# Kernel optimization log

Hardware: AMD Instinct MI355X
Metric: run time of the kernel (lower is better)

Reference implementation:

```python
import jax, jax.numpy as jnp
import numpy as np

N, KS, C = 1_000_000, 9, 16
EPS = 1e-5
SLOPE = 0.2  # LeakyReLU negative_slope


def _leaky(x):
    return jnp.where(x >= 0, x, SLOPE * x)


def _batchnorm(x, gamma, beta):
    # BatchNorm1d in training mode: biased batch statistics over the N axis
    mean = x.mean(axis=0)
    var = x.var(axis=0)
    return gamma * (x - mean) * jax.lax.rsqrt(var + EPS) + beta


def setup_inputs() -> dict:
    key = jax.random.key(0)
    k = jax.random.split(key, 5)
    xav = (2.0 / (C + C)) ** 0.5  # xavier-normal-ish scale for [C_in, C_out, ks]
    return {
        "data": jax.random.normal(k[0], (N, C), jnp.float32),
        "ind": jax.random.randint(k[1], (N, KS), 0, N),
        "w1": jax.random.normal(k[2], (C, C, KS), jnp.float32) * xav,
        "b1": jax.random.normal(k[3], (C,), jnp.float32) * 0.01,
        "gamma1": jnp.ones((C,), jnp.float32),
        "beta1": jnp.zeros((C,), jnp.float32),
        "w2": jax.random.normal(k[4], (C, C, KS), jnp.float32) * xav,
        "gamma2": jnp.ones((C,), jnp.float32),
        "beta2": jnp.zeros((C,), jnp.float32),
    }


def reference(data, ind, w1, b1, gamma1, beta1, w2, gamma2, beta2):
    # gather neighborhoods: [N, ks, C]
    inp = data[ind]
    # torch.einsum('ijk,klj->il', data[N,ks,C], weight[C,Cout,ks]) -> [N, Cout]
    out = jnp.einsum('njc,coj->no', inp, w1) + b1
    out = _leaky(_batchnorm(out, gamma1, beta1))
    # second gather + tree-conv, no bias
    out = jnp.einsum('njc,coj->no', out[ind], w2)
    out = _batchnorm(out, gamma2, beta2)
    # residual (in_channels == out_channels -> identity shortcut)
    return _leaky(out + data)
```

## Files before the change

### kernel.cpp

```cpp
#include <hip/hip_runtime.h>

typedef unsigned int uint;
typedef unsigned short ushort;

#define NN 1000000
#define KSZ 9
#define CH 16
#define KTOT 144
#define NBLK 1024
#define TILES64 15625

typedef float f32x4 __attribute__((ext_vector_type(4)));
typedef short s16x8 __attribute__((ext_vector_type(8)));

__device__ __forceinline__ float bf2f(ushort v) { return __uint_as_float(((uint)v) << 16); }
__device__ __forceinline__ ushort f2bf(float f) {
  uint u = __float_as_uint(f);
  return (ushort)((u + 0x7fffu + ((u >> 16) & 1u)) >> 16);
}
__device__ __forceinline__ float leaky(float x) { return x >= 0.f ? x : 0.2f * x; }

__global__ __launch_bounds__(256)
void k_cast(const float* __restrict__ in, ushort* __restrict__ out) {
  size_t i0 = ((size_t)blockIdx.x * 256 + (size_t)threadIdx.x) * 8;
  if (i0 >= (size_t)NN * CH) return;
  float4 a = *(const float4*)(in + i0);
  float4 b = *(const float4*)(in + i0 + 4);
  float e[8] = {a.x, a.y, a.z, a.w, b.x, b.y, b.z, b.w};
  uint pk[4];
#pragma unroll
  for (int p = 0; p < 4; ++p)
    pk[p] = (uint)f2bf(e[2*p]) | ((uint)f2bf(e[2*p+1]) << 16);
  *(uint4*)(out + i0) = *(uint4*)pk;
}

template<bool BN>
__global__ __launch_bounds__(256)
void k_conv(const ushort* __restrict__ src, const int* __restrict__ ind,
            const float* __restrict__ w, const float* __restrict__ bias,
            const float* __restrict__ statsIn, const float* __restrict__ gamma,
            const float* __restrict__ beta,
            ushort* __restrict__ outv, float* __restrict__ accumOut) {
  const int lane = threadIdx.x & 63;
  const int wid  = threadIdx.x >> 6;
  const int o = lane & 15;
  const int q = lane >> 4;
  const int qh = q >> 1;
  const int ch0 = (q & 1) * 8;

  __shared__ int   idxs[4][160];
  __shared__ float red[4][32];
  __shared__ float dsc[16], dsh[16];

  s16x8 bfrag[5];
#pragma unroll
  for (int t = 0; t < 5; ++t) {
#pragma unroll
    for (int i = 0; i < 8; ++i) {
      int k = t * 32 + q * 8 + i;
      ushort wv = 0;
      if (k < KTOT) { int j = k >> 4, c = k & 15; wv = f2bf(w[(c * CH + o) * KSZ + j]); }
      bfrag[t][i] = (short)wv;
    }
  }

  float bo = 0.f;
  float sc8[8], sh8[8];
  if constexpr (BN) {
    if (threadIdx.x < 16) {
      int c = threadIdx.x;
      float s = statsIn[c], sq = statsIn[16 + c];
      float mean = s * (1.0f / NN);
      float var  = sq * (1.0f / NN) - mean * mean;
      float scale = gamma[c] * rsqrtf(var + 1e-5f);
      dsc[c] = scale; dsh[c] = beta[c] - mean * scale;
    }
    __syncthreads();
#pragma unroll
    for (int i = 0; i < 8; ++i) { sc8[i] = dsc[ch0 + i]; sh8[i] = dsh[ch0 + i]; }
  } else {
    bo = bias[o];
  }

  int* idxw = idxs[wid];
  float wsum = 0.f, wsq = 0.f;

  for (int g = blockIdx.x; g < TILES64; g += NBLK) {
    const int base  = g * 64 + wid * 16;
    const int base9 = base * 9;

    {
      int r = lane;            idxw[r] = ind[base9 + r];
      r = lane + 64;           idxw[r] = ind[base9 + r];
      r = lane + 128; if (r < KTOT) idxw[r] = ind[base9 + r];
    }

    int i0 = idxw[o * KSZ + (0 + qh)];
    int i1 = idxw[o * KSZ + (2 + qh)];
    int i2 = idxw[o * KSZ + (4 + qh)];
    int i3 = idxw[o * KSZ + (6 + qh)];
    int i4 = idxw[o * KSZ + 8];

    const ushort* p0 = src + (size_t)i0 * CH + ch0;
    const ushort* p1 = src + (size_t)i1 * CH + ch0;
    const ushort* p2 = src + (size_t)i2 * CH + ch0;
    const ushort* p3 = src + (size_t)i3 * CH + ch0;
    const ushort* p4 = src + (size_t)i4 * CH + ch0;

    s16x8 ld0, ld1, ld2, ld3, ld4;
    asm volatile("global_load_dwordx4 %0, %1, off sc0" : "=&v"(ld0) : "v"(p0) : "memory");
    asm volatile("global_load_dwordx4 %0, %1, off sc0" : "=&v"(ld1) : "v"(p1) : "memory");
    asm volatile("global_load_dwordx4 %0, %1, off sc0" : "=&v"(ld2) : "v"(p2) : "memory");
    asm volatile("global_load_dwordx4 %0, %1, off sc0" : "=&v"(ld3) : "v"(p3) : "memory");
    asm volatile("global_load_dwordx4 %0, %1, off sc0" : "=&v"(ld4) : "v"(p4) : "memory");
    asm volatile("s_waitcnt vmcnt(0)" ::: "memory");
    __builtin_amdgcn_sched_barrier(0);

    s16x8 a0, a1, a2, a3, a4;
    if constexpr (BN) {
      auto xf = [&](s16x8 v) -> s16x8 {
        s16x8 r;
#pragma unroll
        for (int i = 0; i < 8; ++i) {
          float x = bf2f((ushort)v[i]);
          r[i] = (short)f2bf(leaky(sc8[i] * x + sh8[i]));
        }
        return r;
      };
      a0 = xf(ld0); a1 = xf(ld1); a2 = xf(ld2); a3 = xf(ld3); a4 = xf(ld4);
    } else {
      a0 = ld0; a1 = ld1; a2 = ld2; a3 = ld3; a4 = ld4;
    }
    if (qh) { s16x8 z = {0,0,0,0,0,0,0,0}; a4 = z; }

    f32x4 acc = {0.f, 0.f, 0.f, 0.f};
    acc = __builtin_amdgcn_mfma_f32_16x16x32_bf16(a0, bfrag[0], acc, 0, 0, 0);
    acc = __builtin_amdgcn_mfma_f32_16x16x32_bf16(a1, bfrag[1], acc, 0, 0, 0);
    acc = __builtin_amdgcn_mfma_f32_16x16x32_bf16(a2, bfrag[2], acc, 0, 0, 0);
    acc = __builtin_amdgcn_mfma_f32_16x16x32_bf16(a3, bfrag[3], acc, 0, 0, 0);
    acc = __builtin_amdgcn_mfma_f32_16x16x32_bf16(a4, bfrag[4], acc, 0, 0, 0);

#pragma unroll
    for (int r = 0; r < 4; ++r) {
      float v = acc[r] + bo;
      ushort hv = f2bf(v);
      outv[(size_t)(base + q * 4 + r) * CH + o] = hv;
      float vr = bf2f(hv);
      wsum += vr;
      wsq  += vr * vr;
    }
  }

  wsum += __shfl_xor(wsum, 16);  wsum += __shfl_xor(wsum, 32);
  wsq  += __shfl_xor(wsq, 16);   wsq  += __shfl_xor(wsq, 32);
  if (lane < 16) { red[wid][lane] = wsum; red[wid][16 + lane] = wsq; }
  __syncthreads();
  if (threadIdx.x < 32) {
    float s = red[0][threadIdx.x] + red[1][threadIdx.x] + red[2][threadIdx.x] + red[3][threadIdx.x];
    atomicAdd(&accumOut[threadIdx.x], s);
  }
}

__global__ __launch_bounds__(256)
void k_final(const ushort* __restrict__ o2, const float* __restrict__ data,
             const float* __restrict__ statsIn, const float* __restrict__ gamma,
             const float* __restrict__ beta, float* __restrict__ out) {
  __shared__ float dsc[16], dsh[16];
  if (threadIdx.x < 16) {
    int c = threadIdx.x;
    float s = statsIn[c], sq = statsIn[16 + c];
    float mean = s * (1.0f / NN);
    float var  = sq * (1.0f / NN) - mean * mean;
    float scale = gamma[c] * rsqrtf(var + 1e-5f);
    dsc[c] = scale; dsh[c] = beta[c] - mean * scale;
  }
  __syncthreads();
  size_t t = (size_t)blockIdx.x * 256 + threadIdx.x;
  size_t i0 = t * 8;
  if (i0 >= (size_t)NN * CH) return;
  int coff = (int)(i0 & 15);
  float sc[8], sh[8];
#pragma unroll
  for (int p = 0; p < 8; ++p) { sc[p] = dsc[coff + p]; sh[p] = dsh[coff + p]; }
  uint4 a = *(const uint4*)(o2 + i0);
  float4 d0 = *(const float4*)(data + i0);
  float4 d1 = *(const float4*)(data + i0 + 4);
  uint ua[4] = {a.x, a.y, a.z, a.w};
  float dd[8] = {d0.x, d0.y, d0.z, d0.w, d1.x, d1.y, d1.z, d1.w};
  float y[8];
#pragma unroll
  for (int p = 0; p < 4; ++p) {
    float x0 = __uint_as_float(ua[p] << 16);
    float x1 = __uint_as_float(ua[p] & 0xffff0000u);
    y[2*p]   = leaky(sc[2*p]   * x0 + sh[2*p]   + dd[2*p]);
    y[2*p+1] = leaky(sc[2*p+1] * x1 + sh[2*p+1] + dd[2*p+1]);
  }
  float4 r0 = {y[0], y[1], y[2], y[3]};
  float4 r1 = {y[4], y[5], y[6], y[7]};
  *(float4*)(out + i0) = r0;
  *(float4*)(out + i0 + 4) = r1;
}

extern "C" void kernel_launch(void* const* d_in, const int* in_sizes, int n_in,
                              void* d_out, int out_size, void* d_ws, size_t ws_size,
                              hipStream_t stream) {
  const float* data   = (const float*)d_in[0];
  const int*   ind    = (const int*)d_in[1];
  const float* w1     = (const float*)d_in[2];
  const float* b1     = (const float*)d_in[3];
  const float* gamma1 = (const float*)d_in[4];
  const float* beta1  = (const float*)d_in[5];
  const float* w2     = (const float*)d_in[6];
  const float* gamma2 = (const float*)d_in[7];
  const float* beta2  = (const float*)d_in[8];
  float* out = (float*)d_out;

  ushort* out1  = (ushort*)d_out;
  ushort* dataB = out1 + (size_t)NN * CH;
  float*  accum1 = (float*)d_ws;
  float*  accum2 = accum1 + 32;
  ushort* out2   = (ushort*)((char*)d_ws + 256);

  hipMemsetAsync(d_ws, 0, 256, stream);

  hipLaunchKernelGGL(k_cast, dim3((NN * CH / 8 + 255) / 256), dim3(256), 0, stream,
                     data, dataB);
  hipLaunchKernelGGL((k_conv<false>), dim3(NBLK), dim3(256), 0, stream,
                     dataB, ind, w1, b1,
                     (const float*)nullptr, (const float*)nullptr, (const float*)nullptr,
                     out1, accum1);
  hipLaunchKernelGGL((k_conv<true>), dim3(NBLK), dim3(256), 0, stream,
                     out1, ind, w2, (const float*)nullptr,
                     accum1, gamma1, beta1,
                     out2, accum2);
  hipLaunchKernelGGL(k_final, dim3((NN * CH / 8 + 255) / 256), dim3(256), 0, stream,
                     out2, data, accum2, gamma2, beta2, out);
}
```

Before: 471.6 us.

## Partition gathers into index-range passes with soft grid barriers for cache locality

Each conv kernel now caches all of a block's tile indices in shared memory and keeps 16 accumulators per wave. It sweeps the source array in 8 index-range windows (index >> 17), with a bounded-spin soft barrier across blocks before each pass. Each pass only loads the gathered rows that fall in the current window, so the working set of random gathers can stay in L2/MALL. The BN+leaky transform on layer-1 output moves out of the second conv into a separate in-place elementwise kernel, so the conv is one template again. In exchange, every tile is revisited 8 times, register pressure rises, barrier spinning costs time, and there is an extra pass over the intermediate tensor.

Result: slower. 1.256 ms (+166.3%).

```diff
diff --git a/kernel.cpp b/kernel.cpp
--- a/kernel.cpp
+++ b/kernel.cpp
@@ -9,6 +9,9 @@
 #define KTOT 144
 #define NBLK 1024
 #define TILES64 15625
+#define MAXT 16
+#define WSHIFT 17
+#define NPASS 8
 
 typedef float f32x4 __attribute__((ext_vector_type(4)));
 typedef short s16x8 __attribute__((ext_vector_type(8)));
@@ -19,6 +22,18 @@
   return (ushort)((u + 0x7fffu + ((u >> 16) & 1u)) >> 16);
 }
 __device__ __forceinline__ float leaky(float x) { return x >= 0.f ? x : 0.2f * x; }
+
+__device__ __forceinline__ void soft_barrier(int* bar, int wp) {
+  __syncthreads();
+  if (threadIdx.x == 0) {
+    __hip_atomic_fetch_add(&bar[wp], 1, __ATOMIC_RELAXED, __HIP_MEMORY_SCOPE_AGENT);
+    int tries = 0;
+    while (__hip_atomic_load(&bar[wp], __ATOMIC_RELAXED, __HIP_MEMORY_SCOPE_AGENT) < NBLK
+           && ++tries < 96)
+      __builtin_amdgcn_s_sleep(8);
+  }
+  __syncthreads();
+}
 
 __global__ __launch_bounds__(256)
 void k_cast(const float* __restrict__ in, ushort* __restrict__ out) {
@@ -34,13 +49,11 @@
   *(uint4*)(out + i0) = *(uint4*)pk;
 }
 
-template<bool BN>
-__global__ __launch_bounds__(256)
+__global__ __launch_bounds__(256, 4)
 void k_conv(const ushort* __restrict__ src, const int* __restrict__ ind,
             const float* __restrict__ w, const float* __restrict__ bias,
-            const float* __restrict__ statsIn, const float* __restrict__ gamma,
-            const float* __restrict__ beta,
-            ushort* __restrict__ outv, float* __restrict__ accumOut) {
+            ushort* __restrict__ outv, float* __restrict__ accumOut,
+            int* __restrict__ bar) {
   const int lane = threadIdx.x & 63;
   const int wid  = threadIdx.x >> 6;
   const int o = lane & 15;
@@ -48,9 +61,8 @@
   const int qh = q >> 1;
   const int ch0 = (q & 1) * 8;
 
-  __shared__ int   idxs[4][160];
+  __shared__ int   idxs[4][MAXT][KTOT];
   __shared__ float red[4][32];
-  __shared__ float dsc[16], dsh[16];
 
   s16x8 bfrag[5];
 #pragma unroll
@@ -64,85 +76,67 @@
     }
   }
 
-  float bo = 0.f;
-  float sc8[8], sh8[8];
-  if constexpr (BN) {
-    if (threadIdx.x < 16) {
-      int c = threadIdx.x;
-      float s = statsIn[c], sq = statsIn[16 + c];
-      float mean = s * (1.0f / NN);
-      float var  = sq * (1.0f / NN) - mean * mean;
-      float scale = gamma[c] * rsqrtf(var + 1e-5f);
-      dsc[c] = scale; dsh[c] = beta[c] - mean * scale;
-    }
-    __syncthreads();
-#pragma unroll
-    for (int i = 0; i < 8; ++i) { sc8[i] = dsc[ch0 + i]; sh8[i] = dsh[ch0 + i]; }
-  } else {
-    bo = bias[o];
-  }
-
-  int* idxw = idxs[wid];
+  float bo = bias ? bias[o] : 0.f;
+
+#pragma unroll
+  for (int tt = 0; tt < MAXT; ++tt) {
+    int g = blockIdx.x + tt * NBLK;
+    if (g < TILES64) {
+      int base9 = (g * 64 + wid * 16) * 9;
+      idxs[wid][tt][lane]      = ind[base9 + lane];
+      idxs[wid][tt][lane + 64] = ind[base9 + lane + 64];
+      if (lane < KTOT - 128) idxs[wid][tt][lane + 128] = ind[base9 + lane + 128];
+    }
+  }
+
+  f32x4 acc[MAXT];
+#pragma unroll
+  for (int tt = 0; tt < MAXT; ++tt) acc[tt] = (f32x4){0.f, 0.f, 0.f, 0.f};
+
+  for (int wp = 0; wp < NPASS; ++wp) {
+    soft_barrier(bar, wp);
+#pragma unroll
+    for (int tt = 0; tt < MAXT; ++tt) {
+      int g = blockIdx.x + tt * NBLK;
+      if (g >= TILES64) continue;
+      const int* tix = idxs[wid][tt];
+      int i0 = tix[o * KSZ + 0 + qh];
+      int i1 = tix[o * KSZ + 2 + qh];
+      int i2 = tix[o * KSZ + 4 + qh];
+      int i3 = tix[o * KSZ + 6 + qh];
+      int i4 = tix[o * KSZ + 8];
+      const ushort* p0 = src + (size_t)i0 * CH + ch0;
+      const ushort* p1 = src + (size_t)i1 * CH + ch0;
+      const ushort* p2 = src + (size_t)i2 * CH + ch0;
+      const ushort* p3 = src + (size_t)i3 * CH + ch0;
+      const ushort* p4 = src + (size_t)i4 * CH + ch0;
+      s16x8 z = {0,0,0,0,0,0,0,0};
+      s16x8 a0 = z, a1 = z, a2 = z, a3 = z, a4 = z;
+      if ((i0 >> WSHIFT) == wp) asm volatile("global_load_dwordx4 %0, %1, off sc0" : "+v"(a0) : "v"(p0) : "memory");
+      if ((i1 >> WSHIFT) == wp) asm volatile("global_load_dwordx4 %0, %1, off sc0" : "+v"(a1) : "v"(p1) : "memory");
+      if ((i2 >> WSHIFT) == wp) asm volatile("global_load_dwordx4 %0, %1, off sc0" : "+v"(a2) : "v"(p2) : "memory");
+      if ((i3 >> WSHIFT) == wp) asm volatile("global_load_dwordx4 %0, %1, off sc0" : "+v"(a3) : "v"(p3) : "memory");
+      if (qh == 0 && (i4 >> WSHIFT) == wp)
+        asm volatile("global_load_dwordx4 %0, %1, off sc0" : "+v"(a4) : "v"(p4) : "memory");
+      asm volatile("s_waitcnt vmcnt(0)" ::: "memory");
+      __builtin_amdgcn_sched_barrier(0);
+      acc[tt] = __builtin_amdgcn_mfma_f32_16x16x32_bf16(a0, bfrag[0], acc[tt], 0, 0, 0);
+      acc[tt] = __builtin_amdgcn_mfma_f32_16x16x32_bf16(a1, bfrag[1], acc[tt], 0, 0, 0);
+      acc[tt] = __builtin_amdgcn_mfma_f32_16x16x32_bf16(a2, bfrag[2], acc[tt], 0, 0, 0);
+      acc[tt] = __builtin_amdgcn_mfma_f32_16x16x32_bf16(a3, bfrag[3], acc[tt], 0, 0, 0);
+      acc[tt] = __builtin_amdgcn_mfma_f32_16x16x32_bf16(a4, bfrag[4], acc[tt], 0, 0, 0);
+    }
+  }
+
   float wsum = 0.f, wsq = 0.f;
-
-  for (int g = blockIdx.x; g < TILES64; g += NBLK) {
-    const int base  = g * 64 + wid * 16;
-    const int base9 = base * 9;
-
-    {
-      int r = lane;            idxw[r] = ind[base9 + r];
-      r = lane + 64;           idxw[r] = ind[base9 + r];
-      r = lane + 128; if (r < KTOT) idxw[r] = ind[base9 + r];
-    }
-
-    int i0 = idxw[o * KSZ + (0 + qh)];
-    int i1 = idxw[o * KSZ + (2 + qh)];
-    int i2 = idxw[o * KSZ + (4 + qh)];
-    int i3 = idxw[o * KSZ + (6 + qh)];
-    int i4 = idxw[o * KSZ + 8];
-
-    const ushort* p0 = src + (size_t)i0 * CH + ch0;
-    const ushort* p1 = src + (size_t)i1 * CH + ch0;
-    const ushort* p2 = src + (size_t)i2 * CH + ch0;
-    const ushort* p3 = src + (size_t)i3 * CH + ch0;
-    const ushort* p4 = src + (size_t)i4 * CH + ch0;
-
-    s16x8 ld0, ld1, ld2, ld3, ld4;
-    asm volatile("global_load_dwordx4 %0, %1, off sc0" : "=&v"(ld0) : "v"(p0) : "memory");
-    asm volatile("global_load_dwordx4 %0, %1, off sc0" : "=&v"(ld1) : "v"(p1) : "memory");
-    asm volatile("global_load_dwordx4 %0, %1, off sc0" : "=&v"(ld2) : "v"(p2) : "memory");
-    asm volatile("global_load_dwordx4 %0, %1, off sc0" : "=&v"(ld3) : "v"(p3) : "memory");
-    asm volatile("global_load_dwordx4 %0, %1, off sc0" : "=&v"(ld4) : "v"(p4) : "memory");
-    asm volatile("s_waitcnt vmcnt(0)" ::: "memory");
-    __builtin_amdgcn_sched_barrier(0);
-
-    s16x8 a0, a1, a2, a3, a4;
-    if constexpr (BN) {
-      auto xf = [&](s16x8 v) -> s16x8 {
-        s16x8 r;
-#pragma unroll
-        for (int i = 0; i < 8; ++i) {
-          float x = bf2f((ushort)v[i]);
-          r[i] = (short)f2bf(leaky(sc8[i] * x + sh8[i]));
-        }
-        return r;
-      };
-      a0 = xf(ld0); a1 = xf(ld1); a2 = xf(ld2); a3 = xf(ld3); a4 = xf(ld4);
-    } else {
-      a0 = ld0; a1 = ld1; a2 = ld2; a3 = ld3; a4 = ld4;
-    }
-    if (qh) { s16x8 z = {0,0,0,0,0,0,0,0}; a4 = z; }
-
-    f32x4 acc = {0.f, 0.f, 0.f, 0.f};
-    acc = __builtin_amdgcn_mfma_f32_16x16x32_bf16(a0, bfrag[0], acc, 0, 0, 0);
-    acc = __builtin_amdgcn_mfma_f32_16x16x32_bf16(a1, bfrag[1], acc, 0, 0, 0);
-    acc = __builtin_amdgcn_mfma_f32_16x16x32_bf16(a2, bfrag[2], acc, 0, 0, 0);
-    acc = __builtin_amdgcn_mfma_f32_16x16x32_bf16(a3, bfrag[3], acc, 0, 0, 0);
-    acc = __builtin_amdgcn_mfma_f32_16x16x32_bf16(a4, bfrag[4], acc, 0, 0, 0);
-
+#pragma unroll
+  for (int tt = 0; tt < MAXT; ++tt) {
+    int g = blockIdx.x + tt * NBLK;
+    if (g >= TILES64) continue;
+    int base = g * 64 + wid * 16;
 #pragma unroll
     for (int r = 0; r < 4; ++r) {
-      float v = acc[r] + bo;
+      float v = acc[tt][r] + bo;
       ushort hv = f2bf(v);
       outv[(size_t)(base + q * 4 + r) * CH + o] = hv;
       float vr = bf2f(hv);
@@ -159,6 +153,39 @@
     float s = red[0][threadIdx.x] + red[1][threadIdx.x] + red[2][threadIdx.x] + red[3][threadIdx.x];
     atomicAdd(&accumOut[threadIdx.x], s);
   }
+}
+
+__global__ __launch_bounds__(256)
+void k_bn(ushort* __restrict__ io, const float* __restrict__ statsIn,
+          const float* __restrict__ gamma, const float* __restrict__ beta) {
+  __shared__ float dsc[16], dsh[16];
+  if (threadIdx.x < 16) {
+    int c = threadIdx.x;
+    float s = statsIn[c], sq = statsIn[16 + c];
+    float mean = s * (1.0f / NN);
+    float var  = sq * (1.0f / NN) - mean * mean;
+    float scale = gamma[c] * rsqrtf(var + 1e-5f);
+    dsc[c] = scale; dsh[c] = beta[c] - mean * scale;
+  }
+  __syncthreads();
+  size_t i0 = ((size_t)blockIdx.x * 256 + (size_t)threadIdx.x) * 8;
+  if (i0 >= (size_t)NN * CH) return;
+  int coff = (int)(i0 & 15);
+  float sc[8], sh[8];
+#pragma unroll
+  for (int p = 0; p < 8; ++p) { sc[p] = dsc[coff + p]; sh[p] = dsh[coff + p]; }
+  uint4 a = *(const uint4*)(io + i0);
+  uint ua[4] = {a.x, a.y, a.z, a.w};
+  uint pk[4];
+#pragma unroll
+  for (int p = 0; p < 4; ++p) {
+    float x0 = __uint_as_float(ua[p] << 16);
+    float x1 = __uint_as_float(ua[p] & 0xffff0000u);
+    float y0 = leaky(sc[2*p]   * x0 + sh[2*p]);
+    float y1 = leaky(sc[2*p+1] * x1 + sh[2*p+1]);
+    pk[p] = (uint)f2bf(y0) | ((uint)f2bf(y1) << 16);
+  }
+  *(uint4*)(io + i0) = *(uint4*)pk;
 }
 
 __global__ __launch_bounds__(256)
@@ -219,20 +246,24 @@
   ushort* dataB = out1 + (size_t)NN * CH;
   float*  accum1 = (float*)d_ws;
   float*  accum2 = accum1 + 32;
-  ushort* out2   = (ushort*)((char*)d_ws + 256);
-
-  hipMemsetAsync(d_ws, 0, 256, stream);
+  int*    bar1   = (int*)((char*)d_ws + 256);
+  int*    bar2   = bar1 + 8;
+  ushort* out2   = (ushort*)((char*)d_ws + 4096);
+
+  hipMemsetAsync(d_ws, 0, 512, stream);
 
   hipLaunchKernelGGL(k_cast, dim3((NN * CH / 8 + 255) / 256), dim3(256), 0, stream,
                      data, dataB);
-  hipLaunchKernelGGL((k_conv<false>), dim3(NBLK), dim3(256), 0, stream,
-                     dataB, ind, w1, b1,
-                     (const float*)nullptr, (const float*)nullptr, (const float*)nullptr,
-                     out1, accum1);
-  hipLaunchKernelGGL((k_conv<true>), dim3(NBLK), dim3(256), 0, stream,
-                     out1, ind, w2, (const float*)nullptr,
-                     accum1, gamma1, beta1,
-                     out2, accum2);
+
+  hipLaunchKernelGGL(k_conv, dim3(NBLK), dim3(256), 0, stream,
+                     dataB, ind, w1, b1, out1, accum1, bar1);
+
+  hipLaunchKernelGGL(k_bn, dim3((NN * CH / 8 + 255) / 256), dim3(256), 0, stream,
+                     out1, accum1, gamma1, beta1);
+
+  hipLaunchKernelGGL(k_conv, dim3(NBLK), dim3(256), 0, stream,
+                     out1, ind, w2, (const float*)nullptr, out2, accum2, bar2);
+
   hipLaunchKernelGGL(k_final, dim3((NN * CH / 8 + 255) / 256), dim3(256), 0, stream,
                      out2, data, accum2, gamma2, beta2, out);
 }
```

## Fuse fp32-to-bf16 cast into first conv gather and double block count

Applied to the files above, without the earlier changes.

Drops the separate cast kernel. The first conv now gathers the fp32 rows directly, using two 16-byte loads per neighbor, and packs them to bf16 with v_cvt_pk_bf16_f32 in registers. This removes one full pass over the input and the write of a bf16 copy, but the first conv's random gathers now move twice as many bytes. The grid-stride block count is also raised from 1024 to 2048, and the out2 workspace offset moves to 4096.

Result: no change. 471.2 us (-0.1%).

```diff
diff --git a/kernel.cpp b/kernel.cpp
--- a/kernel.cpp
+++ b/kernel.cpp
@@ -7,7 +7,7 @@
 #define KSZ 9
 #define CH 16
 #define KTOT 144
-#define NBLK 1024
+#define NBLK 2048
 #define TILES64 15625
 
 typedef float f32x4 __attribute__((ext_vector_type(4)));
@@ -20,23 +20,9 @@
 }
 __device__ __forceinline__ float leaky(float x) { return x >= 0.f ? x : 0.2f * x; }
 
+template<bool FP32SRC>
 __global__ __launch_bounds__(256)
-void k_cast(const float* __restrict__ in, ushort* __restrict__ out) {
-  size_t i0 = ((size_t)blockIdx.x * 256 + (size_t)threadIdx.x) * 8;
-  if (i0 >= (size_t)NN * CH) return;
-  float4 a = *(const float4*)(in + i0);
-  float4 b = *(const float4*)(in + i0 + 4);
-  float e[8] = {a.x, a.y, a.z, a.w, b.x, b.y, b.z, b.w};
-  uint pk[4];
-#pragma unroll
-  for (int p = 0; p < 4; ++p)
-    pk[p] = (uint)f2bf(e[2*p]) | ((uint)f2bf(e[2*p+1]) << 16);
-  *(uint4*)(out + i0) = *(uint4*)pk;
-}
-
-template<bool BN>
-__global__ __launch_bounds__(256)
-void k_conv(const ushort* __restrict__ src, const int* __restrict__ ind,
+void k_conv(const void* __restrict__ srcv, const int* __restrict__ ind,
             const float* __restrict__ w, const float* __restrict__ bias,
             const float* __restrict__ statsIn, const float* __restrict__ gamma,
             const float* __restrict__ beta,
@@ -47,6 +33,7 @@
   const int q = lane >> 4;
   const int qh = q >> 1;
   const int ch0 = (q & 1) * 8;
+  const int o9 = o * KSZ;
 
   __shared__ int   idxs[4][160];
   __shared__ float red[4][32];
@@ -66,7 +53,9 @@
 
   float bo = 0.f;
   float sc8[8], sh8[8];
-  if constexpr (BN) {
+  if constexpr (FP32SRC) {
+    bo = bias[o];
+  } else {
     if (threadIdx.x < 16) {
       int c = threadIdx.x;
       float s = statsIn[c], sq = statsIn[16 + c];
@@ -78,8 +67,6 @@
     __syncthreads();
 #pragma unroll
     for (int i = 0; i < 8; ++i) { sc8[i] = dsc[ch0 + i]; sh8[i] = dsh[ch0 + i]; }
-  } else {
-    bo = bias[o];
   }
 
   int* idxw = idxs[wid];
@@ -89,35 +76,63 @@
     const int base  = g * 64 + wid * 16;
     const int base9 = base * 9;
 
-    {
-      int r = lane;            idxw[r] = ind[base9 + r];
-      r = lane + 64;           idxw[r] = ind[base9 + r];
-      r = lane + 128; if (r < KTOT) idxw[r] = ind[base9 + r];
-    }
-
-    int i0 = idxw[o * KSZ + (0 + qh)];
-    int i1 = idxw[o * KSZ + (2 + qh)];
-    int i2 = idxw[o * KSZ + (4 + qh)];
-    int i3 = idxw[o * KSZ + (6 + qh)];
-    int i4 = idxw[o * KSZ + 8];
-
-    const ushort* p0 = src + (size_t)i0 * CH + ch0;
-    const ushort* p1 = src + (size_t)i1 * CH + ch0;
-    const ushort* p2 = src + (size_t)i2 * CH + ch0;
-    const ushort* p3 = src + (size_t)i3 * CH + ch0;
-    const ushort* p4 = src + (size_t)i4 * CH + ch0;
-
-    s16x8 ld0, ld1, ld2, ld3, ld4;
-    asm volatile("global_load_dwordx4 %0, %1, off sc0" : "=&v"(ld0) : "v"(p0) : "memory");
-    asm volatile("global_load_dwordx4 %0, %1, off sc0" : "=&v"(ld1) : "v"(p1) : "memory");
-    asm volatile("global_load_dwordx4 %0, %1, off sc0" : "=&v"(ld2) : "v"(p2) : "memory");
-    asm volatile("global_load_dwordx4 %0, %1, off sc0" : "=&v"(ld3) : "v"(p3) : "memory");
-    asm volatile("global_load_dwordx4 %0, %1, off sc0" : "=&v"(ld4) : "v"(p4) : "memory");
-    asm volatile("s_waitcnt vmcnt(0)" ::: "memory");
-    __builtin_amdgcn_sched_barrier(0);
+    idxw[lane]      = ind[base9 + lane];
+    idxw[lane + 64] = ind[base9 + lane + 64];
+    if (lane < KTOT - 128) idxw[lane + 128] = ind[base9 + lane + 128];
+
+    int i0 = idxw[o9 + 0 + qh];
+    int i1 = idxw[o9 + 2 + qh];
+    int i2 = idxw[o9 + 4 + qh];
+    int i3 = idxw[o9 + 6 + qh];
+    int i4 = idxw[o9 + 8];
 
     s16x8 a0, a1, a2, a3, a4;
-    if constexpr (BN) {
+    if constexpr (FP32SRC) {
+      const float* fsrc = (const float*)srcv;
+      const float* p0 = fsrc + (size_t)i0 * CH + ch0;
+      const float* p1 = fsrc + (size_t)i1 * CH + ch0;
+      const float* p2 = fsrc + (size_t)i2 * CH + ch0;
+      const float* p3 = fsrc + (size_t)i3 * CH + ch0;
+      const float* p4 = fsrc + (size_t)i4 * CH + ch0;
+      f32x4 l0a, l0b, l1a, l1b, l2a, l2b, l3a, l3b, l4a, l4b;
+      asm volatile("global_load_dwordx4 %0, %1, off sc0"           : "=&v"(l0a) : "v"(p0) : "memory");
+      asm volatile("global_load_dwordx4 %0, %1, off offset:16 sc0" : "=&v"(l0b) : "v"(p0) : "memory");
+      asm volatile("global_load_dwordx4 %0, %1, off sc0"           : "=&v"(l1a) : "v"(p1) : "memory");
+      asm volatile("global_load_dwordx4 %0, %1, off offset:16 sc0" : "=&v"(l1b) : "v"(p1) : "memory");
+      asm volatile("global_load_dwordx4 %0, %1, off sc0"           : "=&v"(l2a) : "v"(p2) : "memory");
+      asm volatile("global_load_dwordx4 %0, %1, off offset:16 sc0" : "=&v"(l2b) : "v"(p2) : "memory");
+      asm volatile("global_load_dwordx4 %0, %1, off sc0"           : "=&v"(l3a) : "v"(p3) : "memory");
+      asm volatile("global_load_dwordx4 %0, %1, off offset:16 sc0" : "=&v"(l3b) : "v"(p3) : "memory");
+      asm volatile("global_load_dwordx4 %0, %1, off sc0"           : "=&v"(l4a) : "v"(p4) : "memory");
+      asm volatile("global_load_dwordx4 %0, %1, off offset:16 sc0" : "=&v"(l4b) : "v"(p4) : "memory");
+      asm volatile("s_waitcnt vmcnt(0)" ::: "memory");
+      __builtin_amdgcn_sched_barrier(0);
+      auto pack = [](f32x4 lo, f32x4 hi) -> s16x8 {
+        uint u0, u1, u2, u3;
+        asm("v_cvt_pk_bf16_f32 %0, %1, %2" : "=v"(u0) : "v"(lo[0]), "v"(lo[1]));
+        asm("v_cvt_pk_bf16_f32 %0, %1, %2" : "=v"(u1) : "v"(lo[2]), "v"(lo[3]));
+        asm("v_cvt_pk_bf16_f32 %0, %1, %2" : "=v"(u2) : "v"(hi[0]), "v"(hi[1]));
+        asm("v_cvt_pk_bf16_f32 %0, %1, %2" : "=v"(u3) : "v"(hi[2]), "v"(hi[3]));
+        uint4 uu = {u0, u1, u2, u3};
+        return *(s16x8*)&uu;
+      };
+      a0 = pack(l0a, l0b); a1 = pack(l1a, l1b); a2 = pack(l2a, l2b);
+      a3 = pack(l3a, l3b); a4 = pack(l4a, l4b);
+    } else {
+      const ushort* bsrc = (const ushort*)srcv;
+      const ushort* p0 = bsrc + (size_t)i0 * CH + ch0;
+      const ushort* p1 = bsrc + (size_t)i1 * CH + ch0;
+      const ushort* p2 = bsrc + (size_t)i2 * CH + ch0;
+      const ushort* p3 = bsrc + (size_t)i3 * CH + ch0;
+      const ushort* p4 = bsrc + (size_t)i4 * CH + ch0;
+      s16x8 ld0, ld1, ld2, ld3, ld4;
+      asm volatile("global_load_dwordx4 %0, %1, off sc0" : "=&v"(ld0) : "v"(p0) : "memory");
+      asm volatile("global_load_dwordx4 %0, %1, off sc0" : "=&v"(ld1) : "v"(p1) : "memory");
+      asm volatile("global_load_dwordx4 %0, %1, off sc0" : "=&v"(ld2) : "v"(p2) : "memory");
+      asm volatile("global_load_dwordx4 %0, %1, off sc0" : "=&v"(ld3) : "v"(p3) : "memory");
+      asm volatile("global_load_dwordx4 %0, %1, off sc0" : "=&v"(ld4) : "v"(p4) : "memory");
+      asm volatile("s_waitcnt vmcnt(0)" ::: "memory");
+      __builtin_amdgcn_sched_barrier(0);
       auto xf = [&](s16x8 v) -> s16x8 {
         s16x8 r;
 #pragma unroll
@@ -128,8 +143,6 @@
         return r;
       };
       a0 = xf(ld0); a1 = xf(ld1); a2 = xf(ld2); a3 = xf(ld3); a4 = xf(ld4);
-    } else {
-      a0 = ld0; a1 = ld1; a2 = ld2; a3 = ld3; a4 = ld4;
     }
     if (qh) { s16x8 z = {0,0,0,0,0,0,0,0}; a4 = z; }
 
@@ -215,24 +228,23 @@
   const float* beta2  = (const float*)d_in[8];
   float* out = (float*)d_out;
 
-  ushort* out1  = (ushort*)d_out;
-  ushort* dataB = out1 + (size_t)NN * CH;
+  ushort* out1 = (ushort*)d_out;
   float*  accum1 = (float*)d_ws;
   float*  accum2 = accum1 + 32;
-  ushort* out2   = (ushort*)((char*)d_ws + 256);
+  ushort* out2   = (ushort*)((char*)d_ws + 4096);
 
   hipMemsetAsync(d_ws, 0, 256, stream);
 
-  hipLaunchKernelGGL(k_cast, dim3((NN * CH / 8 + 255) / 256), dim3(256), 0, stream,
-                     data, dataB);
-  hipLaunchKernelGGL((k_conv<false>), dim3(NBLK), dim3(256), 0, stream,
-                     dataB, ind, w1, b1,
+  hipLaunchKernelGGL((k_conv<true>), dim3(NBLK), dim3(256), 0, stream,
+                     (const void*)data, ind, w1, b1,
                      (const float*)nullptr, (const float*)nullptr, (const float*)nullptr,
                      out1, accum1);
-  hipLaunchKernelGGL((k_conv<true>), dim3(NBLK), dim3(256), 0, stream,
-                     out1, ind, w2, (const float*)nullptr,
+
+  hipLaunchKernelGGL((k_conv<false>), dim3(NBLK), dim3(256), 0, stream,
+                     (const void*)out1, ind, w2, (const float*)nullptr,
                      accum1, gamma1, beta1,
                      out2, accum2);
+
   hipLaunchKernelGGL(k_final, dim3((NN * CH / 8 + 255) / 256), dim3(256), 0, stream,
                      out2, data, accum2, gamma2, beta2, out);
 }
```

## Split gathers into two source-index windows with per-tile register accumulators

Applied to the files above, without the earlier changes.

Each conv block now preloads all of its tile indices into shared memory and keeps up to 16 MFMA accumulators in registers. It then makes two passes, each gathering only neighbours whose source row falls in one half of the index range, so the random-access footprint per pass is smaller and more cache-friendly. The memset is folded into the cast kernel and launch bounds request 4 waves per SIMD. In exchange it issues more index checks and masked loads, uses much more LDS and registers per block, and serialises load waits twice per tile.

Measured after the change: 472.3 us. No clear change (+0.2%).

```diff
diff --git a/kernel.cpp b/kernel.cpp
--- a/kernel.cpp
+++ b/kernel.cpp
@@ -9,6 +9,9 @@
 #define KTOT 144
 #define NBLK 1024
 #define TILES64 15625
+#define MAXT 16
+#define WSHIFT 19
+#define NWIN 2
 
 typedef float f32x4 __attribute__((ext_vector_type(4)));
 typedef short s16x8 __attribute__((ext_vector_type(8)));
@@ -21,7 +24,9 @@
 __device__ __forceinline__ float leaky(float x) { return x >= 0.f ? x : 0.2f * x; }
 
 __global__ __launch_bounds__(256)
-void k_cast(const float* __restrict__ in, ushort* __restrict__ out) {
+void k_cast(const float* __restrict__ in, ushort* __restrict__ out,
+            float* __restrict__ accums) {
+  if (blockIdx.x == 0 && threadIdx.x < 64) accums[threadIdx.x] = 0.f;
   size_t i0 = ((size_t)blockIdx.x * 256 + (size_t)threadIdx.x) * 8;
   if (i0 >= (size_t)NN * CH) return;
   float4 a = *(const float4*)(in + i0);
@@ -35,7 +40,7 @@
 }
 
 template<bool BN>
-__global__ __launch_bounds__(256)
+__global__ __launch_bounds__(256, 4)
 void k_conv(const ushort* __restrict__ src, const int* __restrict__ ind,
             const float* __restrict__ w, const float* __restrict__ bias,
             const float* __restrict__ statsIn, const float* __restrict__ gamma,
@@ -47,8 +52,9 @@
   const int q = lane >> 4;
   const int qh = q >> 1;
   const int ch0 = (q & 1) * 8;
-
-  __shared__ int   idxs[4][160];
+  const int o9 = o * KSZ;
+
+  __shared__ int   idxs[4][MAXT][KTOT];
   __shared__ float red[4][32];
   __shared__ float dsc[16], dsh[16];
 
@@ -82,67 +88,88 @@
     bo = bias[o];
   }
 
-  int* idxw = idxs[wid];
+  const int NT = (TILES64 - 1 - blockIdx.x) / NBLK + 1;
+
+#pragma unroll
+  for (int tt = 0; tt < MAXT; ++tt) {
+    if (tt < NT) {
+      int base9 = ((blockIdx.x + tt * NBLK) * 64 + wid * 16) * 9;
+      idxs[wid][tt][lane]      = ind[base9 + lane];
+      idxs[wid][tt][lane + 64] = ind[base9 + lane + 64];
+      if (lane < KTOT - 128) idxs[wid][tt][lane + 128] = ind[base9 + lane + 128];
+    }
+  }
+
+  f32x4 acc[MAXT];
+#pragma unroll
+  for (int tt = 0; tt < MAXT; ++tt) acc[tt] = (f32x4){0.f, 0.f, 0.f, 0.f};
+
+  for (int wp = 0; wp < NWIN; ++wp) {
+#pragma unroll
+    for (int tt = 0; tt < MAXT; ++tt) {
+      if (tt >= NT) continue;
+      const int* tix = &idxs[wid][tt][0];
+      int i0 = tix[o9 + 0 + qh];
+      int i1 = tix[o9 + 2 + qh];
+      int i2 = tix[o9 + 4 + qh];
+      int i3 = tix[o9 + 6 + qh];
+      int i4 = tix[o9 + 8];
+      const bool w0 = (i0 >> WSHIFT) == wp;
+      const bool w1 = (i1 >> WSHIFT) == wp;
+      const bool w2 = (i2 >> WSHIFT) == wp;
+      const bool w3 = (i3 >> WSHIFT) == wp;
+      const bool w4 = (i4 >> WSHIFT) == wp;
+      const ushort* p0 = src + (size_t)i0 * CH + ch0;
+      const ushort* p1 = src + (size_t)i1 * CH + ch0;
+      const ushort* p2 = src + (size_t)i2 * CH + ch0;
+      const ushort* p3 = src + (size_t)i3 * CH + ch0;
+      const ushort* p4 = src + (size_t)i4 * CH + ch0;
+      s16x8 z = {0,0,0,0,0,0,0,0};
+      s16x8 t0 = z, t1 = z, t2 = z, t3 = z, t4 = z;
+      if (w0) asm volatile("global_load_dwordx4 %0, %1, off sc0" : "+v"(t0) : "v"(p0) : "memory");
+      if (w1) asm volatile("global_load_dwordx4 %0, %1, off sc0" : "+v"(t1) : "v"(p1) : "memory");
+      if (w2) asm volatile("global_load_dwordx4 %0, %1, off sc0" : "+v"(t2) : "v"(p2) : "memory");
+      if (w3) asm volatile("global_load_dwordx4 %0, %1, off sc0" : "+v"(t3) : "v"(p3) : "memory");
+      if (qh == 0 && w4)
+        asm volatile("global_load_dwordx4 %0, %1, off sc0" : "+v"(t4) : "v"(p4) : "memory");
+      asm volatile("s_waitcnt vmcnt(0)" ::: "memory");
+      __builtin_amdgcn_sched_barrier(0);
+      s16x8 a0, a1, a2, a3, a4;
+      if constexpr (BN) {
+        auto xf = [&](s16x8 v) -> s16x8 {
+          s16x8 r;
+#pragma unroll
+          for (int i = 0; i < 8; ++i) {
+            float x = bf2f((ushort)v[i]);
+            r[i] = (short)f2bf(leaky(sc8[i] * x + sh8[i]));
+          }
+          return r;
+        };
+        a0 = w0 ? xf(t0) : z;
+        a1 = w1 ? xf(t1) : z;
+        a2 = w2 ? xf(t2) : z;
+        a3 = w3 ? xf(t3) : z;
+        a4 = w4 ? xf(t4) : z;
+      } else {
+        a0 = t0; a1 = t1; a2 = t2; a3 = t3; a4 = t4;
+      }
+      if (qh) a4 = z;
+      acc[tt] = __builtin_amdgcn_mfma_f32_16x16x32_bf16(a0, bfrag[0], acc[tt], 0, 0, 0);
+      acc[tt] = __builtin_amdgcn_mfma_f32_16x16x32_bf16(a1, bfrag[1], acc[tt], 0, 0, 0);
+      acc[tt] = __builtin_amdgcn_mfma_f32_16x16x32_bf16(a2, bfrag[2], acc[tt], 0, 0, 0);
+      acc[tt] = __builtin_amdgcn_mfma_f32_16x16x32_bf16(a3, bfrag[3], acc[tt], 0, 0, 0);
+      acc[tt] = __builtin_amdgcn_mfma_f32_16x16x32_bf16(a4, bfrag[4], acc[tt], 0, 0, 0);
+    }
+  }
+
   float wsum = 0.f, wsq = 0.f;
-
-  for (int g = blockIdx.x; g < TILES64; g += NBLK) {
-    const int base  = g * 64 + wid * 16;
-    const int base9 = base * 9;
-
-    {
-      int r = lane;            idxw[r] = ind[base9 + r];
-      r = lane + 64;           idxw[r] = ind[base9 + r];
-      r = lane + 128; if (r < KTOT) idxw[r] = ind[base9 + r];
-    }
-
-    int i0 = idxw[o * KSZ + (0 + qh)];
-    int i1 = idxw[o * KSZ + (2 + qh)];
-    int i2 = idxw[o * KSZ + (4 + qh)];
-    int i3 = idxw[o * KSZ + (6 + qh)];
-    int i4 = idxw[o * KSZ + 8];
-
-    const ushort* p0 = src + (size_t)i0 * CH + ch0;
-    const ushort* p1 = src + (size_t)i1 * CH + ch0;
-    const ushort* p2 = src + (size_t)i2 * CH + ch0;
-    const ushort* p3 = src + (size_t)i3 * CH + ch0;
-    const ushort* p4 = src + (size_t)i4 * CH + ch0;
-
-    s16x8 ld0, ld1, ld2, ld3, ld4;
-    asm volatile("global_load_dwordx4 %0, %1, off sc0" : "=&v"(ld0) : "v"(p0) : "memory");
-    asm volatile("global_load_dwordx4 %0, %1, off sc0" : "=&v"(ld1) : "v"(p1) : "memory");
-    asm volatile("global_load_dwordx4 %0, %1, off sc0" : "=&v"(ld2) : "v"(p2) : "memory");
-    asm volatile("global_load_dwordx4 %0, %1, off sc0" : "=&v"(ld3) : "v"(p3) : "memory");
-    asm volatile("global_load_dwordx4 %0, %1, off sc0" : "=&v"(ld4) : "v"(p4) : "memory");
-    asm volatile("s_waitcnt vmcnt(0)" ::: "memory");
-    __builtin_amdgcn_sched_barrier(0);
-
-    s16x8 a0, a1, a2, a3, a4;
-    if constexpr (BN) {
-      auto xf = [&](s16x8 v) -> s16x8 {
-        s16x8 r;
-#pragma unroll
-        for (int i = 0; i < 8; ++i) {
-          float x = bf2f((ushort)v[i]);
-          r[i] = (short)f2bf(leaky(sc8[i] * x + sh8[i]));
-        }
-        return r;
-      };
-      a0 = xf(ld0); a1 = xf(ld1); a2 = xf(ld2); a3 = xf(ld3); a4 = xf(ld4);
-    } else {
-      a0 = ld0; a1 = ld1; a2 = ld2; a3 = ld3; a4 = ld4;
-    }
-    if (qh) { s16x8 z = {0,0,0,0,0,0,0,0}; a4 = z; }
-
-    f32x4 acc = {0.f, 0.f, 0.f, 0.f};
-    acc = __builtin_amdgcn_mfma_f32_16x16x32_bf16(a0, bfrag[0], acc, 0, 0, 0);
-    acc = __builtin_amdgcn_mfma_f32_16x16x32_bf16(a1, bfrag[1], acc, 0, 0, 0);
-    acc = __builtin_amdgcn_mfma_f32_16x16x32_bf16(a2, bfrag[2], acc, 0, 0, 0);
-    acc = __builtin_amdgcn_mfma_f32_16x16x32_bf16(a3, bfrag[3], acc, 0, 0, 0);
-    acc = __builtin_amdgcn_mfma_f32_16x16x32_bf16(a4, bfrag[4], acc, 0, 0, 0);
-
+#pragma unroll
+  for (int tt = 0; tt < MAXT; ++tt) {
+    if (tt >= NT) continue;
+    int base = (blockIdx.x + tt * NBLK) * 64 + wid * 16;
 #pragma unroll
     for (int r = 0; r < 4; ++r) {
-      float v = acc[r] + bo;
+      float v = acc[tt][r] + bo;
       ushort hv = f2bf(v);
       outv[(size_t)(base + q * 4 + r) * CH + o] = hv;
       float vr = bf2f(hv);
@@ -219,20 +246,21 @@
   ushort* dataB = out1 + (size_t)NN * CH;
   float*  accum1 = (float*)d_ws;
   float*  accum2 = accum1 + 32;
-  ushort* out2   = (ushort*)((char*)d_ws + 256);
-
-  hipMemsetAsync(d_ws, 0, 256, stream);
+  ushort* out2   = (ushort*)((char*)d_ws + 4096);
 
   hipLaunchKernelGGL(k_cast, dim3((NN * CH / 8 + 255) / 256), dim3(256), 0, stream,
-                     data, dataB);
+                     data, dataB, accum1);
+
   hipLaunchKernelGGL((k_conv<false>), dim3(NBLK), dim3(256), 0, stream,
                      dataB, ind, w1, b1,
                      (const float*)nullptr, (const float*)nullptr, (const float*)nullptr,
                      out1, accum1);
+
   hipLaunchKernelGGL((k_conv<true>), dim3(NBLK), dim3(256), 0, stream,
                      out1, ind, w2, (const float*)nullptr,
                      accum1, gamma1, beta1,
                      out2, accum2);
+
   hipLaunchKernelGGL(k_final, dim3((NN * CH / 8 + 255) / 256), dim3(256), 0, stream,
                      out2, data, accum2, gamma2, beta2, out);
 }
```
